# Kernel optimization log

Hardware: AMD Instinct MI355X
Metric: run time of the kernel (lower is better)

## Reference

```python
import jax, jax.numpy as jnp
import numpy as np

N, C, H, W = 16, 4, 512, 512
EPS = 1e-06
SMOOTH = 1.0


def _class_weights(target, num_classes):
    # torch loop `for i in range(max+1): mask=(t==i); w += mask/(mask.sum()+eps)`
    # == per-pixel lookup of 1/(global class count + eps). Classes > max never
    # appear so their (huge) weight is multiplied by a zero mask -> identical.
    counts = jnp.zeros((num_classes,), dtype=jnp.float32).at[target.reshape(-1)].add(1.0)
    cw = 1.0 / (counts + EPS)
    return cw[target]  # [n, H, W]


def reference(pred, target):
    n, c, h, w = pred.shape
    # Weighted cross entropy (target clamped to [0, c-1] as in torch code)
    tgt = jnp.clip(target, 0, c - 1)
    weights = _class_weights(tgt, c)  # [n,H,W]
    logp = jax.nn.log_softmax(pred, axis=1)
    logp_t = jnp.take_along_axis(logp, tgt[:, None, :, :], axis=1)[:, 0]  # [n,H,W]
    w_flat = weights.reshape(n, -1)
    wce = -jnp.mean((logp_t * weights).reshape(n, -1).sum(1) / w_flat.sum(1))
    # Dice loss: target integer values used directly (no one-hot), per original
    tf = tgt.astype(pred.dtype)
    tw = tf * weights  # [n,H,W]
    inter = jnp.einsum('nchw,nhw->nc', pred, tw)
    union = jnp.einsum('nchw,nhw->nc', pred, weights) + tw.sum(axis=(1, 2))[:, None]
    dice = jnp.mean(1.0 - (2.0 * inter + SMOOTH) / (union + SMOOTH))
    return wce + dice


def setup_inputs() -> dict:
    key = jax.random.key(0)
    k1, k2 = jax.random.split(key)
    pred = jax.random.normal(k1, (N, C, H, W), dtype=jnp.float32)
    target = jax.random.randint(k2, (N, H, W), 0, C, dtype=jnp.int64)
    return {"pred": pred, "target": target}
```

## Files before the change

### kernel.cpp

```cpp
#include <hip/hip_runtime.h>

#define HW (512 * 512)
#define NB 16
#define NC 4
#define HBLK 1024
#define MBX 64


__global__ __launch_bounds__(256) void hist_kernel(const int* __restrict__ tgt,
                                                   unsigned int* __restrict__ hp,
                                                   int n4) {
    int idx = blockIdx.x * blockDim.x + threadIdx.x;
    int stride = gridDim.x * blockDim.x;
    unsigned int c0 = 0, c1 = 0, c2 = 0, c3 = 0;
    for (int i = idx; i < n4; i += stride) {
        int4 t = reinterpret_cast<const int4*>(tgt)[i];
        int a = min(max(t.x, 0), 3);
        int b = min(max(t.y, 0), 3);
        int c = min(max(t.z, 0), 3);
        int d = min(max(t.w, 0), 3);
        c0 += (a == 0) + (b == 0) + (c == 0) + (d == 0);
        c1 += (a == 1) + (b == 1) + (c == 1) + (d == 1);
        c2 += (a == 2) + (b == 2) + (c == 2) + (d == 2);
        c3 += (a == 3) + (b == 3) + (c == 3) + (d == 3);
    }
#pragma unroll
    for (int o = 32; o >= 1; o >>= 1) {
        c0 += __shfl_down(c0, o);
        c1 += __shfl_down(c1, o);
        c2 += __shfl_down(c2, o);
        c3 += __shfl_down(c3, o);
    }
    __shared__ unsigned int s[4][4];
    int lane = threadIdx.x & 63, wid = threadIdx.x >> 6;
    if (lane == 0) {
        s[wid][0] = c0; s[wid][1] = c1; s[wid][2] = c2; s[wid][3] = c3;
    }
    __syncthreads();
    if (threadIdx.x < 4) {
        hp[blockIdx.x * 4 + threadIdx.x] =
            s[0][threadIdx.x] + s[1][threadIdx.x] + s[2][threadIdx.x] + s[3][threadIdx.x];
    }
}

__global__ __launch_bounds__(256) void main_kernel(const float* __restrict__ pred,
                                                   const int* __restrict__ tgt,
                                                   const unsigned int* __restrict__ hp,
                                                   float* __restrict__ mp) {
    const int n = blockIdx.y;
    const int bx = blockIdx.x;

    unsigned int c[4] = {0, 0, 0, 0};
#pragma unroll
    for (int j = 0; j < HBLK / 256; ++j) {
        int b = threadIdx.x + j * 256;
        uint4 r = reinterpret_cast<const uint4*>(hp)[b];
        c[0] += r.x; c[1] += r.y; c[2] += r.z; c[3] += r.w;
    }
#pragma unroll
    for (int o = 32; o >= 1; o >>= 1) {
#pragma unroll
        for (int k = 0; k < 4; k++) c[k] += __shfl_down(c[k], o);
    }
    __shared__ unsigned int sc[4][4];
    {
        int lane = threadIdx.x & 63, wid = threadIdx.x >> 6;
        if (lane == 0) {
#pragma unroll
            for (int k = 0; k < 4; k++) sc[wid][k] = c[k];
        }
    }
    __syncthreads();
    float cw[4];
#pragma unroll
    for (int k = 0; k < 4; k++)
        cw[k] = 1.0f / ((float)(sc[0][k] + sc[1][k] + sc[2][k] + sc[3][k]) + 1e-6f);

    float s1 = 0.f, s2 = 0.f, tsum = 0.f;
    float inter[4] = {0.f, 0.f, 0.f, 0.f};
    float uni[4] = {0.f, 0.f, 0.f, 0.f};

    const int4* t4p = reinterpret_cast<const int4*>(tgt + (size_t)n * HW);
    const float4* p0 = reinterpret_cast<const float4*>(pred + (size_t)n * NC * HW + 0 * (size_t)HW);
    const float4* p1 = reinterpret_cast<const float4*>(pred + (size_t)n * NC * HW + 1 * (size_t)HW);
    const float4* p2 = reinterpret_cast<const float4*>(pred + (size_t)n * NC * HW + 2 * (size_t)HW);
    const float4* p3 = reinterpret_cast<const float4*>(pred + (size_t)n * NC * HW + 3 * (size_t)HW);

    int i0 = bx * blockDim.x + threadIdx.x;
    const int stride4 = MBX * 256;
#pragma unroll
    for (int it = 0; it < (HW / 4) / (MBX * 256); ++it) {
        int i = i0 + it * stride4;
        int4 t4 = t4p[i];
        float4 a = p0[i];
        float4 b = p1[i];
        float4 cc = p2[i];
        float4 d = p3[i];
        int tt[4] = {t4.x, t4.y, t4.z, t4.w};
        float va[4] = {a.x, a.y, a.z, a.w};
        float vb[4] = {b.x, b.y, b.z, b.w};
        float vc[4] = {cc.x, cc.y, cc.z, cc.w};
        float vd[4] = {d.x, d.y, d.z, d.w};
#pragma unroll
        for (int j = 0; j < 4; ++j) {
            int t = min(max(tt[j], 0), 3);
            float w = (t == 0) ? cw[0] : (t == 1) ? cw[1] : (t == 2) ? cw[2] : cw[3];
            float x0 = va[j], x1 = vb[j], x2 = vc[j], x3 = vd[j];
            float m = fmaxf(fmaxf(x0, x1), fmaxf(x2, x3));
            float e = __expf(x0 - m) + __expf(x1 - m) + __expf(x2 - m) + __expf(x3 - m);
            float lse = __logf(e) + m;
            float pt = (t == 0) ? x0 : (t == 1) ? x1 : (t == 2) ? x2 : x3;
            float logp_t = pt - lse;
            float tw = (float)t * w;
            s1 += logp_t * w;
            s2 += w;
            tsum += tw;
            inter[0] += x0 * tw; uni[0] += x0 * w;
            inter[1] += x1 * tw; uni[1] += x1 * w;
            inter[2] += x2 * tw; uni[2] += x2 * w;
            inter[3] += x3 * tw; uni[3] += x3 * w;
        }
    }

    float vals[11] = {s1, s2, tsum, inter[0], inter[1], inter[2], inter[3],
                      uni[0], uni[1], uni[2], uni[3]};
#pragma unroll
    for (int k = 0; k < 11; k++) {
#pragma unroll
        for (int o = 32; o >= 1; o >>= 1) vals[k] += __shfl_down(vals[k], o);
    }
    __shared__ float sred[4][11];
    int lane = threadIdx.x & 63, wid = threadIdx.x >> 6;
    if (lane == 0) {
#pragma unroll
        for (int k = 0; k < 11; k++) sred[wid][k] = vals[k];
    }
    __syncthreads();
    if (threadIdx.x < 11) {
        int k = threadIdx.x;
        mp[(n * MBX + bx) * 11 + k] = sred[0][k] + sred[1][k] + sred[2][k] + sred[3][k];
    }
}

__global__ __launch_bounds__(256) void finalize_kernel(const float* __restrict__ mp,
                                                       float* __restrict__ out) {
    __shared__ float red[NB][11];
    int t = threadIdx.x;
    if (t < NB * 11) {
        int n = t / 11, k = t % 11;
        float s = 0.f;
#pragma unroll 8
        for (int bx = 0; bx < MBX; ++bx) s += mp[(n * MBX + bx) * 11 + k];
        red[n][k] = s;
    }
    __syncthreads();
    if (t < 64) {
        int n = t >> 2, cc = t & 3;
        float T = red[n][2];
        float I = red[n][3 + cc];
        float U = red[n][7 + cc];
        float dice_term = 1.0f - (2.0f * I + 1.0f) / (U + T + 1.0f);
        float wce_term = (t < 16) ? (red[t][0] / red[t][1]) : 0.0f;
#pragma unroll
        for (int o = 32; o >= 1; o >>= 1) {
            dice_term += __shfl_down(dice_term, o);
            wce_term += __shfl_down(wce_term, o);
        }
        if (t == 0) out[0] = -(wce_term / 16.0f) + dice_term / 64.0f;
    }
}

extern "C" void kernel_launch(void* const* d_in, const int* in_sizes, int n_in,
                              void* d_out, int out_size, void* d_ws, size_t ws_size,
                              hipStream_t stream) {
    const float* pred = (const float*)d_in[0];
    const int* tgt = (const int*)d_in[1];
    float* out = (float*)d_out;
    unsigned int* hp = (unsigned int*)d_ws;
    float* mp = (float*)((char*)d_ws + HBLK * 4 * sizeof(unsigned int));

    hist_kernel<<<HBLK, 256, 0, stream>>>(tgt, hp, NB * HW / 4);
    dim3 grid(MBX, NB);
    main_kernel<<<grid, 256, 0, stream>>>(pred, tgt, hp, mp);
    finalize_kernel<<<1, 256, 0, stream>>>(mp, out);
}
```

Before: 114.7 us.

## Eliminate histogram pass by accumulating per-class sums and applying weights in finalize

```diff
diff --git a/kernel.cpp b/kernel.cpp
--- a/kernel.cpp
+++ b/kernel.cpp
@@ -3,82 +3,23 @@
 #define HW (512 * 512)
 #define NB 16
 #define NC 4
-#define HBLK 1024
 #define MBX 64
+#define NBLK (NB * MBX)
 
-
-__global__ __launch_bounds__(256) void hist_kernel(const int* __restrict__ tgt,
-                                                   unsigned int* __restrict__ hp,
-                                                   int n4) {
-    int idx = blockIdx.x * blockDim.x + threadIdx.x;
-    int stride = gridDim.x * blockDim.x;
-    unsigned int c0 = 0, c1 = 0, c2 = 0, c3 = 0;
-    for (int i = idx; i < n4; i += stride) {
-        int4 t = reinterpret_cast<const int4*>(tgt)[i];
-        int a = min(max(t.x, 0), 3);
-        int b = min(max(t.y, 0), 3);
-        int c = min(max(t.z, 0), 3);
-        int d = min(max(t.w, 0), 3);
-        c0 += (a == 0) + (b == 0) + (c == 0) + (d == 0);
-        c1 += (a == 1) + (b == 1) + (c == 1) + (d == 1);
-        c2 += (a == 2) + (b == 2) + (c == 2) + (d == 2);
-        c3 += (a == 3) + (b == 3) + (c == 3) + (d == 3);
-    }
-#pragma unroll
-    for (int o = 32; o >= 1; o >>= 1) {
-        c0 += __shfl_down(c0, o);
-        c1 += __shfl_down(c1, o);
-        c2 += __shfl_down(c2, o);
-        c3 += __shfl_down(c3, o);
-    }
-    __shared__ unsigned int s[4][4];
-    int lane = threadIdx.x & 63, wid = threadIdx.x >> 6;
-    if (lane == 0) {
-        s[wid][0] = c0; s[wid][1] = c1; s[wid][2] = c2; s[wid][3] = c3;
-    }
-    __syncthreads();
-    if (threadIdx.x < 4) {
-        hp[blockIdx.x * 4 + threadIdx.x] =
-            s[0][threadIdx.x] + s[1][threadIdx.x] + s[2][threadIdx.x] + s[3][threadIdx.x];
-    }
-}
 
 __global__ __launch_bounds__(256) void main_kernel(const float* __restrict__ pred,
                                                    const int* __restrict__ tgt,
-                                                   const unsigned int* __restrict__ hp,
                                                    float* __restrict__ mp) {
     const int n = blockIdx.y;
     const int bx = blockIdx.x;
 
-    unsigned int c[4] = {0, 0, 0, 0};
-#pragma unroll
-    for (int j = 0; j < HBLK / 256; ++j) {
-        int b = threadIdx.x + j * 256;
-        uint4 r = reinterpret_cast<const uint4*>(hp)[b];
-        c[0] += r.x; c[1] += r.y; c[2] += r.z; c[3] += r.w;
-    }
-#pragma unroll
-    for (int o = 32; o >= 1; o >>= 1) {
-#pragma unroll
-        for (int k = 0; k < 4; k++) c[k] += __shfl_down(c[k], o);
-    }
-    __shared__ unsigned int sc[4][4];
-    {
-        int lane = threadIdx.x & 63, wid = threadIdx.x >> 6;
-        if (lane == 0) {
-#pragma unroll
-            for (int k = 0; k < 4; k++) sc[wid][k] = c[k];
-        }
-    }
-    __syncthreads();
-    float cw[4];
+    float cnt[4] = {0.f, 0.f, 0.f, 0.f};
+    float A[4] = {0.f, 0.f, 0.f, 0.f};
+    float B[4][4];
 #pragma unroll
     for (int k = 0; k < 4; k++)
-        cw[k] = 1.0f / ((float)(sc[0][k] + sc[1][k] + sc[2][k] + sc[3][k]) + 1e-6f);
-
-    float s1 = 0.f, s2 = 0.f, tsum = 0.f;
-    float inter[4] = {0.f, 0.f, 0.f, 0.f};
-    float uni[4] = {0.f, 0.f, 0.f, 0.f};
+#pragma unroll
+        for (int c = 0; c < 4; c++) B[k][c] = 0.f;
 
     const int4* t4p = reinterpret_cast<const int4*>(tgt + (size_t)n * HW);
     const float4* p0 = reinterpret_cast<const float4*>(pred + (size_t)n * NC * HW + 0 * (size_t)HW);
@@ -104,63 +45,91 @@
 #pragma unroll
         for (int j = 0; j < 4; ++j) {
             int t = min(max(tt[j], 0), 3);
-            float w = (t == 0) ? cw[0] : (t == 1) ? cw[1] : (t == 2) ? cw[2] : cw[3];
             float x0 = va[j], x1 = vb[j], x2 = vc[j], x3 = vd[j];
             float m = fmaxf(fmaxf(x0, x1), fmaxf(x2, x3));
             float e = __expf(x0 - m) + __expf(x1 - m) + __expf(x2 - m) + __expf(x3 - m);
             float lse = __logf(e) + m;
             float pt = (t == 0) ? x0 : (t == 1) ? x1 : (t == 2) ? x2 : x3;
             float logp_t = pt - lse;
-            float tw = (float)t * w;
-            s1 += logp_t * w;
-            s2 += w;
-            tsum += tw;
-            inter[0] += x0 * tw; uni[0] += x0 * w;
-            inter[1] += x1 * tw; uni[1] += x1 * w;
-            inter[2] += x2 * tw; uni[2] += x2 * w;
-            inter[3] += x3 * tw; uni[3] += x3 * w;
+#pragma unroll
+            for (int k = 0; k < 4; ++k) {
+                bool hit = (t == k);
+                cnt[k] += hit ? 1.0f : 0.0f;
+                A[k] += hit ? logp_t : 0.0f;
+                B[k][0] += hit ? x0 : 0.0f;
+                B[k][1] += hit ? x1 : 0.0f;
+                B[k][2] += hit ? x2 : 0.0f;
+                B[k][3] += hit ? x3 : 0.0f;
+            }
         }
     }
 
-    float vals[11] = {s1, s2, tsum, inter[0], inter[1], inter[2], inter[3],
-                      uni[0], uni[1], uni[2], uni[3]};
+    float vals[24];
 #pragma unroll
-    for (int k = 0; k < 11; k++) {
+    for (int k = 0; k < 4; k++) {
+        vals[k] = cnt[k];
+        vals[4 + k] = A[k];
+#pragma unroll
+        for (int c = 0; c < 4; c++) vals[8 + 4 * k + c] = B[k][c];
+    }
+#pragma unroll
+    for (int k = 0; k < 24; k++) {
 #pragma unroll
         for (int o = 32; o >= 1; o >>= 1) vals[k] += __shfl_down(vals[k], o);
     }
-    __shared__ float sred[4][11];
+    __shared__ float sred[4][24];
     int lane = threadIdx.x & 63, wid = threadIdx.x >> 6;
     if (lane == 0) {
 #pragma unroll
-        for (int k = 0; k < 11; k++) sred[wid][k] = vals[k];
+        for (int k = 0; k < 24; k++) sred[wid][k] = vals[k];
     }
     __syncthreads();
-    if (threadIdx.x < 11) {
+    if (threadIdx.x < 24) {
         int k = threadIdx.x;
-        mp[(n * MBX + bx) * 11 + k] = sred[0][k] + sred[1][k] + sred[2][k] + sred[3][k];
+        mp[k * NBLK + n * MBX + bx] =
+            sred[0][k] + sred[1][k] + sred[2][k] + sred[3][k];
     }
 }
 
-__global__ __launch_bounds__(256) void finalize_kernel(const float* __restrict__ mp,
+__global__ __launch_bounds__(384) void finalize_kernel(const float* __restrict__ mp,
                                                        float* __restrict__ out) {
-    __shared__ float red[NB][11];
+    __shared__ float red[NB][24];
+    __shared__ float cw_s[4];
     int t = threadIdx.x;
-    if (t < NB * 11) {
-        int n = t / 11, k = t % 11;
-        float s = 0.f;
-#pragma unroll 8
-        for (int bx = 0; bx < MBX; ++bx) s += mp[(n * MBX + bx) * 11 + k];
-        red[n][k] = s;
+    {
+        int n = t / 24, j = t % 24;
+        const float4* src = reinterpret_cast<const float4*>(mp + j * NBLK + n * MBX);
+        float4 s4 = {0.f, 0.f, 0.f, 0.f};
+#pragma unroll
+        for (int q = 0; q < MBX / 4; ++q) {
+            float4 v = src[q];
+            s4.x += v.x; s4.y += v.y; s4.z += v.z; s4.w += v.w;
+        }
+        red[n][j] = (s4.x + s4.y) + (s4.z + s4.w);
+    }
+    __syncthreads();
+    if (t < 4) {
+        float g = 0.f;
+#pragma unroll
+        for (int n = 0; n < NB; n++) g += red[n][t];
+        cw_s[t] = 1.0f / (g + 1e-6f);
     }
     __syncthreads();
     if (t < 64) {
-        int n = t >> 2, cc = t & 3;
-        float T = red[n][2];
-        float I = red[n][3 + cc];
-        float U = red[n][7 + cc];
+        int n = t >> 2, c = t & 3;
+        float cw0 = cw_s[0], cw1 = cw_s[1], cw2 = cw_s[2], cw3 = cw_s[3];
+        float T = 1.f * cw1 * red[n][1] + 2.f * cw2 * red[n][2] + 3.f * cw3 * red[n][3];
+        float I = 1.f * cw1 * red[n][8 + 4 + c] + 2.f * cw2 * red[n][8 + 8 + c] +
+                  3.f * cw3 * red[n][8 + 12 + c];
+        float U = cw0 * red[n][8 + 0 + c] + cw1 * red[n][8 + 4 + c] +
+                  cw2 * red[n][8 + 8 + c] + cw3 * red[n][8 + 12 + c];
         float dice_term = 1.0f - (2.0f * I + 1.0f) / (U + T + 1.0f);
-        float wce_term = (t < 16) ? (red[t][0] / red[t][1]) : 0.0f;
+        float wce_term = 0.0f;
+        if (t < 16) {
+            float S1 = cw0 * red[t][4] + cw1 * red[t][5] + cw2 * red[t][6] + cw3 * red[t][7];
+            float S2 = cw0 * red[t][0] + cw1 * red[t][1] + cw2 * red[t][2] + cw3 * red[t][3];
+            wce_term = S1 / S2;
+        }
 #pragma unroll
         for (int o = 32; o >= 1; o >>= 1) {
             dice_term += __shfl_down(dice_term, o);
@@ -176,11 +145,9 @@
     const float* pred = (const float*)d_in[0];
     const int* tgt = (const int*)d_in[1];
     float* out = (float*)d_out;
-    unsigned int* hp = (unsigned int*)d_ws;
-    float* mp = (float*)((char*)d_ws + HBLK * 4 * sizeof(unsigned int));
+    float* mp = (float*)d_ws;
 
-    hist_kernel<<<HBLK, 256, 0, stream>>>(tgt, hp, NB * HW / 4);
     dim3 grid(MBX, NB);
-    main_kernel<<<grid, 256, 0, stream>>>(pred, tgt, hp, mp);
-    finalize_kernel<<<1, 256, 0, stream>>>(mp, out);
+    main_kernel<<<grid, 256, 0, stream>>>(pred, tgt, mp);
+    finalize_kernel<<<1, 384, 0, stream>>>(mp, out);
 }
```

Result: no change. 113.6 us (-0.9%).
